# Optimization experiments

Measured on AMD Instinct MI355X. Metric: run time of the kernel, lower is better.

Reference implementation:

```python
import jax, jax.numpy as jnp
import numpy as np

D_MODEL = 1024
D_STATE = 16
D_CONV = 3
EXPAND = 2
MLP_RATIO = 4
HEADDIM = 64
D_INNER = EXPAND * D_MODEL            # 2048
NHEADS = D_INNER // HEADDIM           # 32
CONV_DIM = D_INNER + 2 * D_STATE      # x, B, C all go through the depthwise conv
D_IN_PROJ = 2 * D_INNER + 2 * D_STATE + NHEADS


def rmsnorm(x, w, eps=1e-6):
    return x * jax.lax.rsqrt(jnp.mean(x * x, axis=-1, keepdims=True) + eps) * w


def silu(x):
    return x * jax.nn.sigmoid(x)


def causal_depthwise_conv(x, w, b):
    # x: (B, L, C); w: (C, K); b: (C,)  -- causal depthwise conv over L
    B, L, C = x.shape
    K = w.shape[1]
    xp = jnp.pad(x, ((0, 0), (K - 1, 0), (0, 0)))
    out = b
    for k in range(K):  # tiny fixed loop over kernel taps (K=3)
        out = out + w[:, k] * xp[:, k:k + L, :]
    return out


def mamba2(h, W_in, conv_w, conv_b, dt_bias, A_log, D, norm_gate_w, W_out):
    B, L, _ = h.shape
    zxbcdt = h @ W_in  # (B, L, D_IN_PROJ)
    z = zxbcdt[..., :D_INNER]
    xBC = zxbcdt[..., D_INNER:D_INNER + CONV_DIM]
    dt = jax.nn.softplus(zxbcdt[..., D_INNER + CONV_DIM:] + dt_bias)  # (B, L, H)

    xBC = silu(causal_depthwise_conv(xBC, conv_w, conv_b))
    x = xBC[..., :D_INNER].reshape(B, L, NHEADS, HEADDIM)
    Bmat = xBC[..., D_INNER:D_INNER + D_STATE]   # (B, L, N)
    Cmat = xBC[..., D_INNER + D_STATE:]          # (B, L, N)

    A = -jnp.exp(A_log)                          # (H,)
    dA = jnp.exp(dt * A)                         # (B, L, H)
    dBx = jnp.einsum('blhp,bln,blh->blhpn', x, Bmat, dt)  # (B, L, H, P, N)

    def step(state, inp):
        dA_t, dBx_t = inp                        # (B,H), (B,H,P,N)
        state = state * dA_t[:, :, None, None] + dBx_t
        return state, state

    s0 = jnp.zeros((B, NHEADS, HEADDIM, D_STATE), dtype=h.dtype)
    _, states = jax.lax.scan(step, s0,
                             (jnp.moveaxis(dA, 1, 0), jnp.moveaxis(dBx, 1, 0)))
    # states: (L, B, H, P, N)
    y = jnp.einsum('lbhpn,bln->blhp', states, Cmat)
    y = y + D[None, None, :, None] * x
    y = y.reshape(B, L, D_INNER)
    y = rmsnorm(y * silu(z), norm_gate_w, eps=1e-5)  # gated RMSNorm as in Mamba2
    return y @ W_out


def setup_inputs() -> dict:
    key = jax.random.key(0)
    ks = jax.random.split(key, 12)
    f = jnp.float32
    d = {}
    d['x'] = jax.random.normal(ks[0], (2, 2048, D_MODEL), dtype=f)
    d['norm1_w'] = jnp.ones((D_MODEL,), f)
    d['W_in'] = jax.random.normal(ks[1], (D_MODEL, D_IN_PROJ), f) * (D_MODEL ** -0.5)
    d['conv_w'] = jax.random.normal(ks[2], (CONV_DIM, D_CONV), f) * 0.2
    d['conv_b'] = jnp.zeros((CONV_DIM,), f)
    d['dt_bias'] = jnp.log(jnp.expm1(jax.random.uniform(ks[3], (NHEADS,), f, 0.001, 0.1)))
    d['A_log'] = jnp.log(jax.random.uniform(ks[4], (NHEADS,), f, 1.0, 16.0))
    d['D'] = jnp.ones((NHEADS,), f)
    d['norm_gate_w'] = jnp.ones((D_INNER,), f)
    d['W_out'] = jax.random.normal(ks[5], (D_INNER, D_MODEL), f) * (D_INNER ** -0.5)
    d['norm2_w'] = jnp.ones((D_MODEL,), f)
    d['mlp_w1'] = jax.random.normal(ks[6], (D_MODEL, D_MODEL * MLP_RATIO), f) * (D_MODEL ** -0.5)
    d['mlp_b1'] = jnp.zeros((D_MODEL * MLP_RATIO,), f)
    d['mlp_w2'] = jax.random.normal(ks[7], (D_MODEL * MLP_RATIO, D_MODEL), f) * ((D_MODEL * MLP_RATIO) ** -0.5)
    d['mlp_b2'] = jnp.zeros((D_MODEL,), f)
    return d


def reference(x, norm1_w, W_in, conv_w, conv_b, dt_bias, A_log, D,
              norm_gate_w, W_out, norm2_w, mlp_w1, mlp_b1, mlp_w2, mlp_b2):
    h = rmsnorm(x, norm1_w)
    h = mamba2(h, W_in, conv_w, conv_b, dt_bias, A_log, D, norm_gate_w, W_out)
    x = x + h
    h = rmsnorm(x, norm2_w)
    h = silu(h @ mlp_w1 + mlp_b1) @ mlp_w2 + mlp_b2
    return x + h
```

## Files before the change

kernel.cpp:

```cpp
#include <hip/hip_runtime.h>

typedef __bf16 bf16;
typedef __bf16 bf16x4 __attribute__((ext_vector_type(4)));
typedef __bf16 bf16x8 __attribute__((ext_vector_type(8)));
typedef float  f32x4  __attribute__((ext_vector_type(4)));

#define BATCH  2
#define SEQ    2048
#define ROWS   (BATCH*SEQ)
#define DMODEL 1024
#define DINNER 2048
#define DSTATE 16
#define NH     32
#define HD     64
#define CONVD  2080
#define DPROJ  4160
#define DMLP   4096
#define DTOFF  (DINNER + CONVD)
#define CS     64
#define NCHUNK (SEQ/CS)

__device__ __forceinline__ float sigmoidf_(float x) { return 1.f / (1.f + expf(-x)); }

__device__ __forceinline__ float blockSum256(float v) {
    #pragma unroll
    for (int o = 32; o > 0; o >>= 1) v += __shfl_down(v, o);
    __shared__ float sb[4];
    const int tid = threadIdx.x;
    if ((tid & 63) == 0) sb[tid >> 6] = v;
    __syncthreads();
    return sb[0] + sb[1] + sb[2] + sb[3];
}

__device__ __forceinline__ void gload_lds16(const bf16* g, bf16* l) {
    __builtin_amdgcn_global_load_lds((const __attribute__((address_space(1))) void*)g,
                                     (__attribute__((address_space(3))) void*)l, 16, 0, 0);
}

__device__ __forceinline__ int xcd_swz(int orig, int nwg) {
    const int q = nwg >> 3, r = nwg & 7;
    const int x = orig & 7, i = orig >> 3;
    return (x < r ? x * (q + 1) : r * (q + 1) + (x - r) * q) + i;
}

__global__ __launch_bounds__(256) void transpose_k(const float* __restrict__ in,
                                                   bf16* __restrict__ out, int R, int C) {
    __shared__ float t[32][33];
    const int bx = blockIdx.x * 32, by = blockIdx.y * 32;
    const int tx = threadIdx.x, ty = threadIdx.y;
    #pragma unroll
    for (int i = 0; i < 4; ++i)
        t[ty + i * 8][tx] = in[(size_t)(by + ty + i * 8) * C + bx + tx];
    __syncthreads();
    #pragma unroll
    for (int i = 0; i < 4; ++i)
        out[(size_t)(bx + ty + i * 8) * R + by + tx] = (bf16)t[tx][ty + i * 8];
}

template<int EPI>
__global__ __launch_bounds__(256) void gemm_bt(
    const bf16* __restrict__ A, const bf16* __restrict__ BT,
    int M, int N, int K, int nbx, int nby,
    bf16* __restrict__ outb, float* __restrict__ outf,
    const float* __restrict__ bias, const float* __restrict__ resf,
    float* __restrict__ dtout)
{
    __shared__ __align__(16) bf16 As[2][128 * 64];
    __shared__ __align__(16) bf16 Bs[2][128 * 64];
    const int nwg = (int)gridDim.x;
    const int wg  = xcd_swz((int)blockIdx.x, nwg);
    const int bx  = wg % nbx;
    const int t2  = wg / nbx;
    const int by  = t2 % nby;
    const int sl  = t2 / nby;
    const int ns  = nwg / (nbx * nby);
    const int Ks  = K / ns;
    const int kbeg = sl * Ks;

    const int tid  = threadIdx.x;
    const int brow = by * 128;
    const int bcol = bx * 128;
    const int lane = tid & 63;
    const int wid  = tid >> 6;
    const int wm = wid >> 1, wn = wid & 1;
    const int lr = lane & 15, lk = lane >> 4;
    const int X  = lr & 7;
    const int off0 = ((lk) ^ X) * 8;
    const int off1 = ((4 + lk) ^ X) * 8;

    f32x4 acc[4][4] = {};

    size_t aoff[4], boff[4];
    #pragma unroll
    for (int i = 0; i < 4; ++i) {
        const int g = tid + i * 256;
        const int srow = g >> 3;
        const int scol = ((g & 7) ^ (srow & 7)) * 8;
        aoff[i] = (size_t)(brow + srow) * K + scol;
        int bn = bcol + srow; if (bn > N - 1) bn = N - 1;
        boff[i] = (size_t)bn * K + scol;
    }

    auto stage = [&](int buf, int k0) {
        #pragma unroll
        for (int i = 0; i < 4; ++i)
            gload_lds16(A + aoff[i] + k0, As[buf] + (tid + i * 256) * 8);
        #pragma unroll
        for (int i = 0; i < 4; ++i)
            gload_lds16(BT + boff[i] + k0, Bs[buf] + (tid + i * 256) * 8);
    };

    const int nt = Ks >> 6;
    stage(0, kbeg);
    __syncthreads();
    for (int t = 0; t < nt; ++t) {
        const int cur = t & 1;
        if (t + 1 < nt) stage(cur ^ 1, kbeg + (t + 1) * 64);
        #pragma unroll
        for (int kk = 0; kk < 2; ++kk) {
            const int off = kk ? off1 : off0;
            bf16x8 af[4], bfr[4];
            #pragma unroll
            for (int m = 0; m < 4; ++m)
                af[m] = *(const bf16x8*)(As[cur] + (wm * 64 + m * 16 + lr) * 64 + off);
            #pragma unroll
            for (int n = 0; n < 4; ++n)
                bfr[n] = *(const bf16x8*)(Bs[cur] + (wn * 64 + n * 16 + lr) * 64 + off);
            #pragma unroll
            for (int m = 0; m < 4; ++m)
                #pragma unroll
                for (int n = 0; n < 4; ++n)
                    acc[m][n] = __builtin_amdgcn_mfma_f32_16x16x32_bf16(af[m], bfr[n], acc[m][n], 0, 0, 0);
        }
        __syncthreads();
    }

    #pragma unroll
    for (int m = 0; m < 4; ++m) {
        const int grow = brow + wm * 64 + m * 16 + lk * 4;
        #pragma unroll
        for (int n = 0; n < 4; ++n) {
            const int gcol = bcol + wn * 64 + n * 16 + lr;
            if (gcol >= N) continue;
            #pragma unroll
            for (int j = 0; j < 4; ++j) {
                const int row = grow + j;
                float v = acc[m][n][j];
                const size_t idx = (size_t)row * N + gcol;
                if constexpr (EPI == 0) {
                    outb[idx] = (bf16)v;
                    if (gcol >= DTOFF)
                        dtout[(size_t)row * NH + (gcol - DTOFF)] = v;
                } else if constexpr (EPI == 1) {
                    v += bias[gcol];
                    v = v * sigmoidf_(v);
                    outb[idx] = (bf16)v;
                } else if constexpr (EPI == 2) {
                    outf[idx] = v + resf[idx];
                } else if constexpr (EPI == 3) {
                    outf[idx] = v + bias[gcol] + resf[idx];
                } else {
                    outf[(size_t)sl * M * N + idx] = v;
                }
            }
        }
    }
}

template<int WITH_BIAS>
__global__ __launch_bounds__(256) void reduce_k(const float* __restrict__ part,
                                                const float* __restrict__ res,
                                                const float* __restrict__ bias,
                                                float* __restrict__ out, int MN) {
    const int i = (blockIdx.x * 256 + threadIdx.x) * 4;
    if (i >= MN) return;
    const float4 a = *(const float4*)(part + i);
    const float4 b = *(const float4*)(part + (size_t)MN + i);
    const float4 c = *(const float4*)(part + 2 * (size_t)MN + i);
    const float4 d = *(const float4*)(part + 3 * (size_t)MN + i);
    const float4 r = *(const float4*)(res + i);
    float4 o;
    o.x = a.x + b.x + c.x + d.x + r.x;
    o.y = a.y + b.y + c.y + d.y + r.y;
    o.z = a.z + b.z + c.z + d.z + r.z;
    o.w = a.w + b.w + c.w + d.w + r.w;
    if constexpr (WITH_BIAS) {
        const int col = i & (DMODEL - 1);
        o.x += bias[col]; o.y += bias[col + 1]; o.z += bias[col + 2]; o.w += bias[col + 3];
    }
    *(float4*)(out + i) = o;
}

__global__ __launch_bounds__(256) void rmsnorm_k(const float* __restrict__ in,
                                                 const float* __restrict__ w,
                                                 bf16* __restrict__ out, float eps) {
    const int row = blockIdx.x, tid = threadIdx.x;
    const float4 v = *(const float4*)(in + (size_t)row * DMODEL + tid * 4);
    float f[4] = { v.x, v.y, v.z, v.w };
    float ss = f[0]*f[0] + f[1]*f[1] + f[2]*f[2] + f[3]*f[3];
    ss = blockSum256(ss);
    const float scale = rsqrtf(ss * (1.f / DMODEL) + eps);
    const float4 wv = *(const float4*)(w + tid * 4);
    const float wa[4] = { wv.x, wv.y, wv.z, wv.w };
    bf16x4 o;
    #pragma unroll
    for (int j = 0; j < 4; ++j) o[j] = (bf16)(f[j] * scale * wa[j]);
    *(bf16x4*)(out + (size_t)row * DMODEL + tid * 4) = o;
}

__global__ __launch_bounds__(256) void rmsgate_k(const float* __restrict__ y,
                                                 const bf16* __restrict__ zx,
                                                 const float* __restrict__ w,
                                                 bf16* __restrict__ out) {
    const int row = blockIdx.x, tid = threadIdx.x;
    const float* yr = y + (size_t)row * DINNER;
    const bf16*  zr = zx + (size_t)row * DPROJ;
    float vals[8];
    float ss = 0.f;
    #pragma unroll
    for (int i = 0; i < 2; ++i) {
        const float4 yv = *(const float4*)(yr + tid * 8 + i * 4);
        const bf16x4 zv = *(const bf16x4*)(zr + tid * 8 + i * 4);
        const float ya[4] = { yv.x, yv.y, yv.z, yv.w };
        #pragma unroll
        for (int j = 0; j < 4; ++j) {
            const float z = (float)zv[j];
            const float t = ya[j] * (z * sigmoidf_(z));
            vals[i * 4 + j] = t;
            ss += t * t;
        }
    }
    ss = blockSum256(ss);
    const float scale = rsqrtf(ss * (1.f / DINNER) + 1e-5f);
    bf16* orow = out + (size_t)row * DINNER + tid * 8;
    #pragma unroll
    for (int i = 0; i < 2; ++i) {
        bf16x4 o;
        #pragma unroll
        for (int j = 0; j < 4; ++j)
            o[j] = (bf16)(vals[i * 4 + j] * scale * w[tid * 8 + i * 4 + j]);
        *(bf16x4*)(orow + i * 4) = o;
    }
}

__global__ __launch_bounds__(256) void conv_silu_k(const bf16* __restrict__ zx,
                                                   const float* __restrict__ cw,
                                                   const float* __restrict__ cb,
                                                   float* __restrict__ xBC) {
    const int idx = blockIdx.x * 256 + threadIdx.x;
    if (idx >= ROWS * CONVD) return;
    const int c  = idx % CONVD;
    const int bl = idx / CONVD;
    const int l  = bl % SEQ;
    float acc = cb[c];
    const bf16* col = zx + (size_t)bl * DPROJ + DINNER + c;
    if (l >= 2) acc += cw[c * 3 + 0] * (float)col[-2 * DPROJ];
    if (l >= 1) acc += cw[c * 3 + 1] * (float)col[-1 * DPROJ];
    acc += cw[c * 3 + 2] * (float)col[0];
    acc = acc * sigmoidf_(acc);
    xBC[(size_t)bl * CONVD + c] = acc;
}

__global__ __launch_bounds__(256) void dtda_k(const float* __restrict__ dtraw,
                                              const float* __restrict__ dt_bias,
                                              const float* __restrict__ A_log,
                                              float* __restrict__ dtb,
                                              float* __restrict__ dab) {
    const int idx = blockIdx.x * 256 + threadIdx.x;
    if (idx >= ROWS * NH) return;
    const int h = idx & (NH - 1);
    const float raw = dtraw[idx] + dt_bias[h];
    const float dt = raw > 20.f ? raw : log1pf(expf(raw));
    const float dA = expf(-expf(A_log[h]) * dt);
    dtb[idx] = dt;
    dab[idx] = dA;
}

__global__ __launch_bounds__(256) void scan1_k(const float* __restrict__ xBC,
                                               const float* __restrict__ dtb,
                                               const float* __restrict__ dab,
                                               float* __restrict__ Sloc,
                                               float* __restrict__ Pc) {
    const int c = blockIdx.x & (NCHUNK - 1);
    const int h = (blockIdx.x >> 5) & (NH - 1);
    const int b = blockIdx.x >> 10;
    const int tid = threadIdx.x;
    const int p  = tid >> 2;
    const int nq = (tid & 3) * 4;
    const size_t rb = (size_t)b * SEQ + c * CS;
    const float* xrow = xBC + rb * CONVD + h * HD + p;
    const float* Brow = xBC + rb * CONVD + DINNER + nq;
    const float* dtp = dtb + rb * NH + h;
    const float* dap = dab + rb * NH + h;
    float s0 = 0.f, s1 = 0.f, s2 = 0.f, s3 = 0.f, P = 1.f;
    for (int l = 0; l < CS; ++l) {
        const float xv  = xrow[(size_t)l * CONVD];
        const float4 Bv = *(const float4*)(Brow + (size_t)l * CONVD);
        const float dtv = dtp[l * NH];
        const float dav = dap[l * NH];
        const float xdt = xv * dtv;
        s0 = s0 * dav + xdt * Bv.x;
        s1 = s1 * dav + xdt * Bv.y;
        s2 = s2 * dav + xdt * Bv.z;
        s3 = s3 * dav + xdt * Bv.w;
        P *= dav;
    }
    float4* dst = (float4*)(Sloc + (size_t)blockIdx.x * 1024 + tid * 4);
    *dst = make_float4(s0, s1, s2, s3);
    if (tid == 0) Pc[blockIdx.x] = P;
}

__global__ __launch_bounds__(256) void scan2_k(const float* __restrict__ Sloc,
                                               const float* __restrict__ Pc,
                                               float* __restrict__ Sini) {
    const int bh = blockIdx.x;
    const int tid = threadIdx.x;
    const size_t base = (size_t)bh * NCHUNK;
    float c0 = 0.f, c1 = 0.f, c2 = 0.f, c3 = 0.f;
    for (int c = 0; c < NCHUNK; ++c) {
        *(float4*)(Sini + (base + c) * 1024 + tid * 4) = make_float4(c0, c1, c2, c3);
        const float4 sl = *(const float4*)(Sloc + (base + c) * 1024 + tid * 4);
        const float P = Pc[base + c];
        c0 = c0 * P + sl.x;
        c1 = c1 * P + sl.y;
        c2 = c2 * P + sl.z;
        c3 = c3 * P + sl.w;
    }
}

__global__ __launch_bounds__(256) void scan3_k(const float* __restrict__ xBC,
                                               const float* __restrict__ dtb,
                                               const float* __restrict__ dab,
                                               const float* __restrict__ Dp,
                                               const float* __restrict__ Sini,
                                               float* __restrict__ y) {
    const int c = blockIdx.x & (NCHUNK - 1);
    const int h = (blockIdx.x >> 5) & (NH - 1);
    const int b = blockIdx.x >> 10;
    const int tid = threadIdx.x;
    const int p  = tid >> 2;
    const int nq = (tid & 3) * 4;
    const float Dh = Dp[h];
    const size_t rb = (size_t)b * SEQ + c * CS;
    const float* xrow = xBC + rb * CONVD + h * HD + p;
    const float* Brow = xBC + rb * CONVD + DINNER + nq;
    const float* Crow = xBC + rb * CONVD + DINNER + DSTATE + nq;
    const float* dtp = dtb + rb * NH + h;
    const float* dap = dab + rb * NH + h;
    float* yp = y + rb * DINNER + h * HD + p;
    const float4 si = *(const float4*)(Sini + (size_t)blockIdx.x * 1024 + tid * 4);
    float s0 = si.x, s1 = si.y, s2 = si.z, s3 = si.w;
    for (int l = 0; l < CS; ++l) {
        const float xv  = xrow[(size_t)l * CONVD];
        const float4 Bv = *(const float4*)(Brow + (size_t)l * CONVD);
        const float4 Cv = *(const float4*)(Crow + (size_t)l * CONVD);
        const float dtv = dtp[l * NH];
        const float dav = dap[l * NH];
        const float xdt = xv * dtv;
        s0 = s0 * dav + xdt * Bv.x;
        s1 = s1 * dav + xdt * Bv.y;
        s2 = s2 * dav + xdt * Bv.z;
        s3 = s3 * dav + xdt * Bv.w;
        float part = s0 * Cv.x + s1 * Cv.y + s2 * Cv.z + s3 * Cv.w;
        part += __shfl_xor(part, 1);
        part += __shfl_xor(part, 2);
        if ((tid & 3) == 0) yp[(size_t)l * DINNER] = part + Dh * xv;
    }
}

extern "C" void kernel_launch(void* const* d_in, const int* in_sizes, int n_in,
                              void* d_out, int out_size, void* d_ws, size_t ws_size,
                              hipStream_t stream) {
    const float* x       = (const float*)d_in[0];
    const float* n1w     = (const float*)d_in[1];
    const float* W_in    = (const float*)d_in[2];
    const float* conv_w  = (const float*)d_in[3];
    const float* conv_b  = (const float*)d_in[4];
    const float* dt_bias = (const float*)d_in[5];
    const float* A_log   = (const float*)d_in[6];
    const float* Dp      = (const float*)d_in[7];
    const float* ngw     = (const float*)d_in[8];
    const float* W_out   = (const float*)d_in[9];
    const float* n2w     = (const float*)d_in[10];
    const float* w1      = (const float*)d_in[11];
    const float* b1      = (const float*)d_in[12];
    const float* w2      = (const float*)d_in[13];
    const float* b2      = (const float*)d_in[14];
    float* out = (float*)d_out;

    char* p = (char*)d_ws;
    auto alloc = [&](size_t bytes) -> char* {
        char* q = p;
        p += (bytes + 255) & ~(size_t)255;
        return q;
    };
    bf16*  W_inT  = (bf16*) alloc((size_t)DPROJ  * DMODEL * 2);
    bf16*  W_outT = (bf16*) alloc((size_t)DMODEL * DINNER * 2);
    bf16*  w1T    = (bf16*) alloc((size_t)DMLP   * DMODEL * 2);
    bf16*  w2T    = (bf16*) alloc((size_t)DMODEL * DMLP   * 2);
    bf16*  h1     = (bf16*) alloc((size_t)ROWS * DMODEL * 2);
    bf16*  zx     = (bf16*) alloc((size_t)ROWS * DPROJ  * 2);
    float* dtraw  = (float*)alloc((size_t)ROWS * NH * 4);
    float* xBC    = (float*)alloc((size_t)ROWS * CONVD * 4);
    float* dtb    = (float*)alloc((size_t)ROWS * NH * 4);
    float* dab    = (float*)alloc((size_t)ROWS * NH * 4);
    float* ybuf   = (float*)alloc((size_t)ROWS * DINNER * 4);
    bf16*  ynorm  = (bf16*) alloc((size_t)ROWS * DINNER * 2);
    float* x2     = (float*)alloc((size_t)ROWS * DMODEL * 4);
    bf16*  h2     = (bf16*) alloc((size_t)ROWS * DMODEL * 2);
    bf16*  mid    = (bf16*) alloc((size_t)ROWS * DMLP * 2);
    float* Sloc   = (float*)alloc((size_t)BATCH * NH * NCHUNK * 1024 * 4);
    float* Sini   = (float*)alloc((size_t)BATCH * NH * NCHUNK * 1024 * 4);
    float* Pc     = (float*)alloc((size_t)BATCH * NH * NCHUNK * 4);
    float* part   = (float*)zx;
    (void)ws_size; (void)in_sizes; (void)n_in; (void)out_size;

    const dim3 tb(32, 8);
    transpose_k<<<dim3(DPROJ / 32, DMODEL / 32), tb, 0, stream>>>(W_in, W_inT, DMODEL, DPROJ);
    transpose_k<<<dim3(DMODEL / 32, DINNER / 32), tb, 0, stream>>>(W_out, W_outT, DINNER, DMODEL);
    transpose_k<<<dim3(DMLP / 32, DMODEL / 32), tb, 0, stream>>>(w1, w1T, DMODEL, DMLP);
    transpose_k<<<dim3(DMODEL / 32, DMLP / 32), tb, 0, stream>>>(w2, w2T, DMLP, DMODEL);

    rmsnorm_k<<<ROWS, 256, 0, stream>>>(x, n1w, h1, 1e-6f);

    gemm_bt<0><<<33 * 32, 256, 0, stream>>>(
        h1, W_inT, ROWS, DPROJ, DMODEL, 33, 32, zx, nullptr, nullptr, nullptr, dtraw);

    conv_silu_k<<<(ROWS * CONVD + 255) / 256, 256, 0, stream>>>(zx, conv_w, conv_b, xBC);
    dtda_k<<<(ROWS * NH + 255) / 256, 256, 0, stream>>>(dtraw, dt_bias, A_log, dtb, dab);

    scan1_k<<<BATCH * NH * NCHUNK, 256, 0, stream>>>(xBC, dtb, dab, Sloc, Pc);
    scan2_k<<<BATCH * NH, 256, 0, stream>>>(Sloc, Pc, Sini);
    scan3_k<<<BATCH * NH * NCHUNK, 256, 0, stream>>>(xBC, dtb, dab, Dp, Sini, ybuf);

    rmsgate_k<<<ROWS, 256, 0, stream>>>(ybuf, zx, ngw, ynorm);

    gemm_bt<4><<<8 * 32 * 4, 256, 0, stream>>>(
        ynorm, W_outT, ROWS, DMODEL, DINNER, 8, 32, nullptr, part, nullptr, nullptr, nullptr);
    reduce_k<0><<<(ROWS * DMODEL / 4 + 255) / 256, 256, 0, stream>>>(
        part, x, nullptr, x2, ROWS * DMODEL);

    rmsnorm_k<<<ROWS, 256, 0, stream>>>(x2, n2w, h2, 1e-6f);

    gemm_bt<1><<<32 * 32, 256, 0, stream>>>(
        h2, w1T, ROWS, DMLP, DMODEL, 32, 32, mid, nullptr, b1, nullptr, nullptr);

    gemm_bt<4><<<8 * 32 * 4, 256, 0, stream>>>(
        mid, w2T, ROWS, DMODEL, DMLP, 8, 32, nullptr, part, nullptr, nullptr, nullptr);
    reduce_k<1><<<(ROWS * DMODEL / 4 + 255) / 256, 256, 0, stream>>>(
        part, x2, b2, out, ROWS * DMODEL);
}
```

Measured before the change: 361.5 us.

## Use 256x256 block-tile GEMM with 512 threads for large projections

Adds a 256x256-tile GEMM kernel with 8 waves, each computing a 128x64 sub-tile, and uses it for the in-projection, out-projection and both MLP GEMMs. This raises the arithmetic intensity per LDS load. The in-projection is split into a 4096-column part handled by the big-tile kernel and a 64-column tail, covering the dt and B/C columns, handled by the old 128-tile kernel. The larger tiles use 128 KB of LDS and more registers per block. They also reduce the number of workgroups (256 for the 4096-wide GEMMs), which may underfill the 256 CUs and limit occupancy.

Result: no change. 354.5 us (-1.9%).

```diff
diff --git a/kernel.cpp b/kernel.cpp
--- a/kernel.cpp
+++ b/kernel.cpp
@@ -58,15 +58,14 @@
 }
 
 template<int EPI>
-__global__ __launch_bounds__(256) void gemm_bt(
+__global__ __launch_bounds__(512) void gemm256_k(
     const bf16* __restrict__ A, const bf16* __restrict__ BT,
-    int M, int N, int K, int nbx, int nby,
+    int K, int ldN, int colofs, int nbx, int nby,
     bf16* __restrict__ outb, float* __restrict__ outf,
-    const float* __restrict__ bias, const float* __restrict__ resf,
-    float* __restrict__ dtout)
+    const float* __restrict__ bias, size_t pstride)
 {
-    __shared__ __align__(16) bf16 As[2][128 * 64];
-    __shared__ __align__(16) bf16 Bs[2][128 * 64];
+    __shared__ __align__(16) bf16 As[2][256 * 64];
+    __shared__ __align__(16) bf16 Bs[2][256 * 64];
     const int nwg = (int)gridDim.x;
     const int wg  = xcd_swz((int)blockIdx.x, nwg);
     const int bx  = wg % nbx;
@@ -76,6 +75,93 @@
     const int ns  = nwg / (nbx * nby);
     const int Ks  = K / ns;
     const int kbeg = sl * Ks;
+
+    const int tid  = threadIdx.x;
+    const int lane = tid & 63, wid = tid >> 6;
+    const int wm = wid >> 2, wn = wid & 3;
+    const int lr = lane & 15, lk = lane >> 4;
+    const int X  = lr & 7;
+    const int brow = by * 256, bcol = bx * 256;
+
+    size_t aoff[4], boff[4];
+    #pragma unroll
+    for (int i = 0; i < 4; ++i) {
+        const int g = tid + i * 512;
+        const int srow = g >> 3;
+        const int scol = ((g & 7) ^ (srow & 7)) * 8;
+        aoff[i] = (size_t)(brow + srow) * K + scol;
+        boff[i] = (size_t)(bcol + srow) * K + scol;
+    }
+
+    auto stage = [&](int buf, int k0) {
+        #pragma unroll
+        for (int i = 0; i < 4; ++i)
+            gload_lds16(A + aoff[i] + k0, As[buf] + (tid + i * 512) * 8);
+        #pragma unroll
+        for (int i = 0; i < 4; ++i)
+            gload_lds16(BT + boff[i] + k0, Bs[buf] + (tid + i * 512) * 8);
+    };
+
+    f32x4 acc[8][4] = {};
+    const int nt = Ks >> 6;
+    stage(0, kbeg);
+    __syncthreads();
+    for (int t = 0; t < nt; ++t) {
+        const int cur = t & 1;
+        if (t + 1 < nt) stage(cur ^ 1, kbeg + (t + 1) * 64);
+        #pragma unroll
+        for (int kk = 0; kk < 2; ++kk) {
+            const int off = ((kk * 4 + lk) ^ X) * 8;
+            bf16x8 bfr[4];
+            #pragma unroll
+            for (int n = 0; n < 4; ++n)
+                bfr[n] = *(const bf16x8*)(Bs[cur] + (wn * 64 + n * 16 + lr) * 64 + off);
+            #pragma unroll
+            for (int m = 0; m < 8; ++m) {
+                const bf16x8 af = *(const bf16x8*)(As[cur] + (wm * 128 + m * 16 + lr) * 64 + off);
+                #pragma unroll
+                for (int n = 0; n < 4; ++n)
+                    acc[m][n] = __builtin_amdgcn_mfma_f32_16x16x32_bf16(af, bfr[n], acc[m][n], 0, 0, 0);
+            }
+        }
+        __syncthreads();
+    }
+
+    #pragma unroll
+    for (int m = 0; m < 8; ++m) {
+        const int grow = brow + wm * 128 + m * 16 + lk * 4;
+        #pragma unroll
+        for (int n = 0; n < 4; ++n) {
+            const int gcol = colofs + bcol + wn * 64 + n * 16 + lr;
+            #pragma unroll
+            for (int j = 0; j < 4; ++j) {
+                const int row = grow + j;
+                float v = acc[m][n][j];
+                if constexpr (EPI == 0) {
+                    outb[(size_t)row * ldN + gcol] = (bf16)v;
+                } else if constexpr (EPI == 1) {
+                    v += bias[gcol];
+                    outb[(size_t)row * ldN + gcol] = (bf16)(v * sigmoidf_(v));
+                } else {
+                    outf[pstride * sl + (size_t)row * ldN + gcol] = v;
+                }
+            }
+        }
+    }
+}
+
+template<int EPI>
+__global__ __launch_bounds__(256) void gemm_bt(
+    const bf16* __restrict__ A, const bf16* __restrict__ BT,
+    int M, int N, int K, int nbx, int nby, int ldN, int colofs,
+    bf16* __restrict__ outb, float* __restrict__ dtout)
+{
+    __shared__ __align__(16) bf16 As[2][128 * 64];
+    __shared__ __align__(16) bf16 Bs[2][128 * 64];
+    const int nwg = (int)gridDim.x;
+    const int wg  = xcd_swz((int)blockIdx.x, nwg);
+    const int bx  = wg % nbx;
+    const int by  = (wg / nbx) % nby;
 
     const int tid  = threadIdx.x;
     const int brow = by * 128;
@@ -110,12 +196,12 @@
             gload_lds16(BT + boff[i] + k0, Bs[buf] + (tid + i * 256) * 8);
     };
 
-    const int nt = Ks >> 6;
-    stage(0, kbeg);
+    const int nt = K >> 6;
+    stage(0, 0);
     __syncthreads();
     for (int t = 0; t < nt; ++t) {
         const int cur = t & 1;
-        if (t + 1 < nt) stage(cur ^ 1, kbeg + (t + 1) * 64);
+        if (t + 1 < nt) stage(cur ^ 1, (t + 1) * 64);
         #pragma unroll
         for (int kk = 0; kk < 2; ++kk) {
             const int off = kk ? off1 : off0;
@@ -145,23 +231,11 @@
             #pragma unroll
             for (int j = 0; j < 4; ++j) {
                 const int row = grow + j;
-                float v = acc[m][n][j];
-                const size_t idx = (size_t)row * N + gcol;
-                if constexpr (EPI == 0) {
-                    outb[idx] = (bf16)v;
-                    if (gcol >= DTOFF)
-                        dtout[(size_t)row * NH + (gcol - DTOFF)] = v;
-                } else if constexpr (EPI == 1) {
-                    v += bias[gcol];
-                    v = v * sigmoidf_(v);
-                    outb[idx] = (bf16)v;
-                } else if constexpr (EPI == 2) {
-                    outf[idx] = v + resf[idx];
-                } else if constexpr (EPI == 3) {
-                    outf[idx] = v + bias[gcol] + resf[idx];
-                } else {
-                    outf[(size_t)sl * M * N + idx] = v;
-                }
+                const float v = acc[m][n][j];
+                const int gc = colofs + gcol;
+                outb[(size_t)row * ldN + gc] = (bf16)v;
+                if (gc >= DTOFF)
+                    dtout[(size_t)row * NH + (gc - DTOFF)] = v;
             }
         }
     }
@@ -413,6 +487,7 @@
     float* Sini   = (float*)alloc((size_t)BATCH * NH * NCHUNK * 1024 * 4);
     float* Pc     = (float*)alloc((size_t)BATCH * NH * NCHUNK * 4);
     float* part   = (float*)zx;
+    const size_t pstride = (size_t)ROWS * DMODEL;
     (void)ws_size; (void)in_sizes; (void)n_in; (void)out_size;
 
     const dim3 tb(32, 8);
@@ -423,8 +498,10 @@
 
     rmsnorm_k<<<ROWS, 256, 0, stream>>>(x, n1w, h1, 1e-6f);
 
-    gemm_bt<0><<<33 * 32, 256, 0, stream>>>(
-        h1, W_inT, ROWS, DPROJ, DMODEL, 33, 32, zx, nullptr, nullptr, nullptr, dtraw);
+    gemm_bt<0><<<32, 256, 0, stream>>>(
+        h1, W_inT + (size_t)4096 * DMODEL, ROWS, 64, DMODEL, 1, 32, DPROJ, 4096, zx, dtraw);
+    gemm256_k<0><<<256, 512, 0, stream>>>(
+        h1, W_inT, DMODEL, DPROJ, 0, 16, 16, zx, nullptr, nullptr, 0);
 
     conv_silu_k<<<(ROWS * CONVD + 255) / 256, 256, 0, stream>>>(zx, conv_w, conv_b, xBC);
     dtda_k<<<(ROWS * NH + 255) / 256, 256, 0, stream>>>(dtraw, dt_bias, A_log, dtb, dab);
@@ -435,18 +512,18 @@
 
     rmsgate_k<<<ROWS, 256, 0, stream>>>(ybuf, zx, ngw, ynorm);
 
-    gemm_bt<4><<<8 * 32 * 4, 256, 0, stream>>>(
-        ynorm, W_outT, ROWS, DMODEL, DINNER, 8, 32, nullptr, part, nullptr, nullptr, nullptr);
+    gemm256_k<2><<<4 * 16 * 4, 512, 0, stream>>>(
+        ynorm, W_outT, DINNER, DMODEL, 0, 4, 16, nullptr, part, nullptr, pstride);
     reduce_k<0><<<(ROWS * DMODEL / 4 + 255) / 256, 256, 0, stream>>>(
         part, x, nullptr, x2, ROWS * DMODEL);
 
     rmsnorm_k<<<ROWS, 256, 0, stream>>>(x2, n2w, h2, 1e-6f);
 
-    gemm_bt<1><<<32 * 32, 256, 0, stream>>>(
-        h2, w1T, ROWS, DMLP, DMODEL, 32, 32, mid, nullptr, b1, nullptr, nullptr);
-
-    gemm_bt<4><<<8 * 32 * 4, 256, 0, stream>>>(
-        mid, w2T, ROWS, DMODEL, DMLP, 8, 32, nullptr, part, nullptr, nullptr, nullptr);
+    gemm256_k<1><<<16 * 16, 512, 0, stream>>>(
+        h2, w1T, DMODEL, DMLP, 0, 16, 16, mid, nullptr, b1, 0);
+
+    gemm256_k<2><<<4 * 16 * 4, 512, 0, stream>>>(
+        mid, w2T, DMLP, DMODEL, 0, 4, 16, nullptr, part, nullptr, pstride);
     reduce_k<1><<<(ROWS * DMODEL / 4 + 255) / 256, 256, 0, stream>>>(
         part, x2, b2, out, ROWS * DMODEL);
 }
```

## Store SSM intermediates in bf16, halve split-K, fuse reduce with RMSNorm

Applied to the files above, without the earlier changes.

The conv output xBC and the scan output y are now stored as bf16 instead of fp32, which halves the memory traffic for the conv, all three scan kernels and the gated norm. The two down-projection GEMMs split K two ways instead of four, so fewer partial buffers are written and read back. The first partial-sum reduction is fused with the second RMSNorm into one per-row kernel. Fewer split-K slices gives less parallelism per GEMM, and bf16 intermediates reduce the precision of the scan inputs.

Measured after the change: 339.8 us. 1.06x faster.

```diff
diff --git a/kernel.cpp b/kernel.cpp
--- a/kernel.cpp
+++ b/kernel.cpp
@@ -19,6 +19,7 @@
 #define DTOFF  (DINNER + CONVD)
 #define CS     64
 #define NCHUNK (SEQ/CS)
+#define NSPLIT 2
 
 __device__ __forceinline__ float sigmoidf_(float x) { return 1.f / (1.f + expf(-x)); }
 
@@ -62,8 +63,7 @@
     const bf16* __restrict__ A, const bf16* __restrict__ BT,
     int M, int N, int K, int nbx, int nby,
     bf16* __restrict__ outb, float* __restrict__ outf,
-    const float* __restrict__ bias, const float* __restrict__ resf,
-    float* __restrict__ dtout)
+    const float* __restrict__ bias, float* __restrict__ dtout, size_t pstride)
 {
     __shared__ __align__(16) bf16 As[2][128 * 64];
     __shared__ __align__(16) bf16 Bs[2][128 * 64];
@@ -146,28 +146,49 @@
             for (int j = 0; j < 4; ++j) {
                 const int row = grow + j;
                 float v = acc[m][n][j];
-                const size_t idx = (size_t)row * N + gcol;
                 if constexpr (EPI == 0) {
-                    outb[idx] = (bf16)v;
+                    outb[(size_t)row * N + gcol] = (bf16)v;
                     if (gcol >= DTOFF)
                         dtout[(size_t)row * NH + (gcol - DTOFF)] = v;
                 } else if constexpr (EPI == 1) {
                     v += bias[gcol];
-                    v = v * sigmoidf_(v);
-                    outb[idx] = (bf16)v;
-                } else if constexpr (EPI == 2) {
-                    outf[idx] = v + resf[idx];
-                } else if constexpr (EPI == 3) {
-                    outf[idx] = v + bias[gcol] + resf[idx];
+                    outb[(size_t)row * N + gcol] = (bf16)(v * sigmoidf_(v));
                 } else {
-                    outf[(size_t)sl * M * N + idx] = v;
+                    outf[pstride * sl + (size_t)row * N + gcol] = v;
                 }
             }
         }
     }
 }
 
-template<int WITH_BIAS>
+__global__ __launch_bounds__(256) void reduce_norm_k(const float* __restrict__ part,
+                                                     const float* __restrict__ res,
+                                                     const float* __restrict__ w,
+                                                     float* __restrict__ x2,
+                                                     bf16* __restrict__ h2) {
+    const int row = blockIdx.x, tid = threadIdx.x;
+    const size_t MN = (size_t)ROWS * DMODEL;
+    const size_t i = (size_t)row * DMODEL + tid * 4;
+    const float4 a = *(const float4*)(part + i);
+    const float4 b = *(const float4*)(part + MN + i);
+    const float4 r = *(const float4*)(res + i);
+    float f[4];
+    f[0] = a.x + b.x + r.x;
+    f[1] = a.y + b.y + r.y;
+    f[2] = a.z + b.z + r.z;
+    f[3] = a.w + b.w + r.w;
+    *(float4*)(x2 + i) = make_float4(f[0], f[1], f[2], f[3]);
+    float ss = f[0]*f[0] + f[1]*f[1] + f[2]*f[2] + f[3]*f[3];
+    ss = blockSum256(ss);
+    const float scale = rsqrtf(ss * (1.f / DMODEL) + 1e-6f);
+    const float4 wv = *(const float4*)(w + tid * 4);
+    const float wa[4] = { wv.x, wv.y, wv.z, wv.w };
+    bf16x4 o;
+    #pragma unroll
+    for (int j = 0; j < 4; ++j) o[j] = (bf16)(f[j] * scale * wa[j]);
+    *(bf16x4*)(h2 + i) = o;
+}
+
 __global__ __launch_bounds__(256) void reduce_k(const float* __restrict__ part,
                                                 const float* __restrict__ res,
                                                 const float* __restrict__ bias,
@@ -176,18 +197,13 @@
     if (i >= MN) return;
     const float4 a = *(const float4*)(part + i);
     const float4 b = *(const float4*)(part + (size_t)MN + i);
-    const float4 c = *(const float4*)(part + 2 * (size_t)MN + i);
-    const float4 d = *(const float4*)(part + 3 * (size_t)MN + i);
     const float4 r = *(const float4*)(res + i);
+    const int col = i & (DMODEL - 1);
     float4 o;
-    o.x = a.x + b.x + c.x + d.x + r.x;
-    o.y = a.y + b.y + c.y + d.y + r.y;
-    o.z = a.z + b.z + c.z + d.z + r.z;
-    o.w = a.w + b.w + c.w + d.w + r.w;
-    if constexpr (WITH_BIAS) {
-        const int col = i & (DMODEL - 1);
-        o.x += bias[col]; o.y += bias[col + 1]; o.z += bias[col + 2]; o.w += bias[col + 3];
-    }
+    o.x = a.x + b.x + r.x + bias[col];
+    o.y = a.y + b.y + r.y + bias[col + 1];
+    o.z = a.z + b.z + r.z + bias[col + 2];
+    o.w = a.w + b.w + r.w + bias[col + 3];
     *(float4*)(out + i) = o;
 }
 
@@ -208,24 +224,23 @@
     *(bf16x4*)(out + (size_t)row * DMODEL + tid * 4) = o;
 }
 
-__global__ __launch_bounds__(256) void rmsgate_k(const float* __restrict__ y,
+__global__ __launch_bounds__(256) void rmsgate_k(const bf16* __restrict__ y,
                                                  const bf16* __restrict__ zx,
                                                  const float* __restrict__ w,
                                                  bf16* __restrict__ out) {
     const int row = blockIdx.x, tid = threadIdx.x;
-    const float* yr = y + (size_t)row * DINNER;
-    const bf16*  zr = zx + (size_t)row * DPROJ;
+    const bf16* yr = y + (size_t)row * DINNER;
+    const bf16* zr = zx + (size_t)row * DPROJ;
     float vals[8];
     float ss = 0.f;
     #pragma unroll
     for (int i = 0; i < 2; ++i) {
-        const float4 yv = *(const float4*)(yr + tid * 8 + i * 4);
+        const bf16x4 yv = *(const bf16x4*)(yr + tid * 8 + i * 4);
         const bf16x4 zv = *(const bf16x4*)(zr + tid * 8 + i * 4);
-        const float ya[4] = { yv.x, yv.y, yv.z, yv.w };
         #pragma unroll
         for (int j = 0; j < 4; ++j) {
             const float z = (float)zv[j];
-            const float t = ya[j] * (z * sigmoidf_(z));
+            const float t = (float)yv[j] * (z * sigmoidf_(z));
             vals[i * 4 + j] = t;
             ss += t * t;
         }
@@ -246,7 +261,7 @@
 __global__ __launch_bounds__(256) void conv_silu_k(const bf16* __restrict__ zx,
                                                    const float* __restrict__ cw,
                                                    const float* __restrict__ cb,
-                                                   float* __restrict__ xBC) {
+                                                   bf16* __restrict__ xBC) {
     const int idx = blockIdx.x * 256 + threadIdx.x;
     if (idx >= ROWS * CONVD) return;
     const int c  = idx % CONVD;
@@ -258,7 +273,7 @@
     if (l >= 1) acc += cw[c * 3 + 1] * (float)col[-1 * DPROJ];
     acc += cw[c * 3 + 2] * (float)col[0];
     acc = acc * sigmoidf_(acc);
-    xBC[(size_t)bl * CONVD + c] = acc;
+    xBC[(size_t)bl * CONVD + c] = (bf16)acc;
 }
 
 __global__ __launch_bounds__(256) void dtda_k(const float* __restrict__ dtraw,
@@ -276,7 +291,7 @@
     dab[idx] = dA;
 }
 
-__global__ __launch_bounds__(256) void scan1_k(const float* __restrict__ xBC,
+__global__ __launch_bounds__(256) void scan1_k(const bf16* __restrict__ xBC,
                                                const float* __restrict__ dtb,
                                                const float* __restrict__ dab,
                                                float* __restrict__ Sloc,
@@ -288,21 +303,21 @@
     const int p  = tid >> 2;
     const int nq = (tid & 3) * 4;
     const size_t rb = (size_t)b * SEQ + c * CS;
-    const float* xrow = xBC + rb * CONVD + h * HD + p;
-    const float* Brow = xBC + rb * CONVD + DINNER + nq;
+    const bf16* xrow = xBC + rb * CONVD + h * HD + p;
+    const bf16* Brow = xBC + rb * CONVD + DINNER + nq;
     const float* dtp = dtb + rb * NH + h;
     const float* dap = dab + rb * NH + h;
     float s0 = 0.f, s1 = 0.f, s2 = 0.f, s3 = 0.f, P = 1.f;
     for (int l = 0; l < CS; ++l) {
-        const float xv  = xrow[(size_t)l * CONVD];
-        const float4 Bv = *(const float4*)(Brow + (size_t)l * CONVD);
+        const float xv  = (float)xrow[(size_t)l * CONVD];
+        const bf16x4 Bv = *(const bf16x4*)(Brow + (size_t)l * CONVD);
         const float dtv = dtp[l * NH];
         const float dav = dap[l * NH];
         const float xdt = xv * dtv;
-        s0 = s0 * dav + xdt * Bv.x;
-        s1 = s1 * dav + xdt * Bv.y;
-        s2 = s2 * dav + xdt * Bv.z;
-        s3 = s3 * dav + xdt * Bv.w;
+        s0 = s0 * dav + xdt * (float)Bv[0];
+        s1 = s1 * dav + xdt * (float)Bv[1];
+        s2 = s2 * dav + xdt * (float)Bv[2];
+        s3 = s3 * dav + xdt * (float)Bv[3];
         P *= dav;
     }
     float4* dst = (float4*)(Sloc + (size_t)blockIdx.x * 1024 + tid * 4);
@@ -328,12 +343,12 @@
     }
 }
 
-__global__ __launch_bounds__(256) void scan3_k(const float* __restrict__ xBC,
+__global__ __launch_bounds__(256) void scan3_k(const bf16* __restrict__ xBC,
                                                const float* __restrict__ dtb,
                                                const float* __restrict__ dab,
                                                const float* __restrict__ Dp,
                                                const float* __restrict__ Sini,
-                                               float* __restrict__ y) {
+                                               bf16* __restrict__ y) {
     const int c = blockIdx.x & (NCHUNK - 1);
     const int h = (blockIdx.x >> 5) & (NH - 1);
     const int b = blockIdx.x >> 10;
@@ -342,29 +357,29 @@
     const int nq = (tid & 3) * 4;
     const float Dh = Dp[h];
     const size_t rb = (size_t)b * SEQ + c * CS;
-    const float* xrow = xBC + rb * CONVD + h * HD + p;
-    const float* Brow = xBC + rb * CONVD + DINNER + nq;
-    const float* Crow = xBC + rb * CONVD + DINNER + DSTATE + nq;
+    const bf16* xrow = xBC + rb * CONVD + h * HD + p;
+    const bf16* Brow = xBC + rb * CONVD + DINNER + nq;
+    const bf16* Crow = xBC + rb * CONVD + DINNER + DSTATE + nq;
     const float* dtp = dtb + rb * NH + h;
     const float* dap = dab + rb * NH + h;
-    float* yp = y + rb * DINNER + h * HD + p;
+    bf16* yp = y + rb * DINNER + h * HD + p;
     const float4 si = *(const float4*)(Sini + (size_t)blockIdx.x * 1024 + tid * 4);
     float s0 = si.x, s1 = si.y, s2 = si.z, s3 = si.w;
     for (int l = 0; l < CS; ++l) {
-        const float xv  = xrow[(size_t)l * CONVD];
-        const float4 Bv = *(const float4*)(Brow + (size_t)l * CONVD);
-        const float4 Cv = *(const float4*)(Crow + (size_t)l * CONVD);
+        const float xv  = (float)xrow[(size_t)l * CONVD];
+        const bf16x4 Bv = *(const bf16x4*)(Brow + (size_t)l * CONVD);
+        const bf16x4 Cv = *(const bf16x4*)(Crow + (size_t)l * CONVD);
         const float dtv = dtp[l * NH];
         const float dav = dap[l * NH];
         const float xdt = xv * dtv;
-        s0 = s0 * dav + xdt * Bv.x;
-        s1 = s1 * dav + xdt * Bv.y;
-        s2 = s2 * dav + xdt * Bv.z;
-        s3 = s3 * dav + xdt * Bv.w;
-        float part = s0 * Cv.x + s1 * Cv.y + s2 * Cv.z + s3 * Cv.w;
+        s0 = s0 * dav + xdt * (float)Bv[0];
+        s1 = s1 * dav + xdt * (float)Bv[1];
+        s2 = s2 * dav + xdt * (float)Bv[2];
+        s3 = s3 * dav + xdt * (float)Bv[3];
+        float part = s0 * (float)Cv[0] + s1 * (float)Cv[1] + s2 * (float)Cv[2] + s3 * (float)Cv[3];
         part += __shfl_xor(part, 1);
         part += __shfl_xor(part, 2);
-        if ((tid & 3) == 0) yp[(size_t)l * DINNER] = part + Dh * xv;
+        if ((tid & 3) == 0) yp[(size_t)l * DINNER] = (bf16)(part + Dh * xv);
     }
 }
 
@@ -401,10 +416,10 @@
     bf16*  h1     = (bf16*) alloc((size_t)ROWS * DMODEL * 2);
     bf16*  zx     = (bf16*) alloc((size_t)ROWS * DPROJ  * 2);
     float* dtraw  = (float*)alloc((size_t)ROWS * NH * 4);
-    float* xBC    = (float*)alloc((size_t)ROWS * CONVD * 4);
+    bf16*  xBC    = (bf16*) alloc((size_t)ROWS * CONVD * 2);
     float* dtb    = (float*)alloc((size_t)ROWS * NH * 4);
     float* dab    = (float*)alloc((size_t)ROWS * NH * 4);
-    float* ybuf   = (float*)alloc((size_t)ROWS * DINNER * 4);
+    bf16*  ybuf   = (bf16*) alloc((size_t)ROWS * DINNER * 2);
     bf16*  ynorm  = (bf16*) alloc((size_t)ROWS * DINNER * 2);
     float* x2     = (float*)alloc((size_t)ROWS * DMODEL * 4);
     bf16*  h2     = (bf16*) alloc((size_t)ROWS * DMODEL * 2);
@@ -413,6 +428,7 @@
     float* Sini   = (float*)alloc((size_t)BATCH * NH * NCHUNK * 1024 * 4);
     float* Pc     = (float*)alloc((size_t)BATCH * NH * NCHUNK * 4);
     float* part   = (float*)zx;
+    const size_t pstride = (size_t)ROWS * DMODEL;
     (void)ws_size; (void)in_sizes; (void)n_in; (void)out_size;
 
     const dim3 tb(32, 8);
@@ -424,7 +440,7 @@
     rmsnorm_k<<<ROWS, 256, 0, stream>>>(x, n1w, h1, 1e-6f);
 
     gemm_bt<0><<<33 * 32, 256, 0, stream>>>(
-        h1, W_inT, ROWS, DPROJ, DMODEL, 33, 32, zx, nullptr, nullptr, nullptr, dtraw);
+        h1, W_inT, ROWS, DPROJ, DMODEL, 33, 32, zx, nullptr, nullptr, dtraw, 0);
 
     conv_silu_k<<<(ROWS * CONVD + 255) / 256, 256, 0, stream>>>(zx, conv_w, conv_b, xBC);
     dtda_k<<<(ROWS * NH + 255) / 256, 256, 0, stream>>>(dtraw, dt_bias, A_log, dtb, dab);
@@ -435,18 +451,15 @@
 
     rmsgate_k<<<ROWS, 256, 0, stream>>>(ybuf, zx, ngw, ynorm);
 
-    gemm_bt<4><<<8 * 32 * 4, 256, 0, stream>>>(
-        ynorm, W_outT, ROWS, DMODEL, DINNER, 8, 32, nullptr, part, nullptr, nullptr, nullptr);
-    reduce_k<0><<<(ROWS * DMODEL / 4 + 255) / 256, 256, 0, stream>>>(
-        part, x, nullptr, x2, ROWS * DMODEL);
-
-    rmsnorm_k<<<ROWS, 256, 0, stream>>>(x2, n2w, h2, 1e-6f);
+    gemm_bt<2><<<8 * 32 * NSPLIT, 256, 0, stream>>>(
+        ynorm, W_outT, ROWS, DMODEL, DINNER, 8, 32, nullptr, part, nullptr, nullptr, pstride);
+    reduce_norm_k<<<ROWS, 256, 0, stream>>>(part, x, n2w, x2, h2);
 
     gemm_bt<1><<<32 * 32, 256, 0, stream>>>(
-        h2, w1T, ROWS, DMLP, DMODEL, 32, 32, mid, nullptr, b1, nullptr, nullptr);
-
-    gemm_bt<4><<<8 * 32 * 4, 256, 0, stream>>>(
-        mid, w2T, ROWS, DMODEL, DMLP, 8, 32, nullptr, part, nullptr, nullptr, nullptr);
-    reduce_k<1><<<(ROWS * DMODEL / 4 + 255) / 256, 256, 0, stream>>>(
+        h2, w1T, ROWS, DMLP, DMODEL, 32, 32, mid, nullptr, b1, nullptr, 0);
+
+    gemm_bt<2><<<8 * 32 * NSPLIT, 256, 0, stream>>>(
+        mid, w2T, ROWS, DMODEL, DMLP, 8, 32, nullptr, part, nullptr, nullptr, pstride);
+    reduce_k<<<(ROWS * DMODEL / 4 + 255) / 256, 256, 0, stream>>>(
         part, x2, b2, out, ROWS * DMODEL);
 }
```
